# Optimization experiments

Hardware: AMD Instinct MI355X
Metric: run time of the kernel (lower is better)

## Reference

```python
import jax, jax.numpy as jnp
import numpy as np

H = 224; W = 224; ZNEAR = 0.01; ZFAR = 100.0; EPS2D = 0.3
N_GAUSS = 1024; N_CAM = 2
ALPHA_MIN = 1.0 / 255.0; ALPHA_MAX = 0.999


def quat_to_rotmat(q):
    # gsplat convention: wxyz, normalized internally. q: [N,4] -> [N,3,3]
    q = q / jnp.linalg.norm(q, axis=-1, keepdims=True)
    w, x, y, z = q[:, 0], q[:, 1], q[:, 2], q[:, 3]
    R = jnp.stack([
        jnp.stack([1.0 - 2.0 * (y * y + z * z), 2.0 * (x * y - w * z), 2.0 * (x * z + w * y)], -1),
        jnp.stack([2.0 * (x * y + w * z), 1.0 - 2.0 * (x * x + z * z), 2.0 * (y * z - w * x)], -1),
        jnp.stack([2.0 * (x * z - w * y), 2.0 * (y * z + w * x), 1.0 - 2.0 * (x * x + y * y)], -1),
    ], -2)
    return R


def setup_inputs() -> dict:
    key = jax.random.key(0)
    ks = jax.random.split(key, 5)
    xyz = jax.random.normal(ks[0], (N_GAUSS, 3), dtype=jnp.float32) * 0.5
    rgb = jax.random.uniform(ks[1], (N_GAUSS, 3), dtype=jnp.float32)
    opacity = jax.random.uniform(ks[2], (N_GAUSS,), dtype=jnp.float32)
    scale = jax.random.uniform(ks[3], (N_GAUSS, 3), dtype=jnp.float32) * 0.04 + 0.005
    rotation = jax.random.normal(ks[4], (N_GAUSS, 4), dtype=jnp.float32)
    w2c_list = []
    for a in (0.0, 0.3):  # two views, small yaw apart, camera 3 units back
        c, s = np.cos(a), np.sin(a)
        w2c_list.append(np.array([[c, 0, -s, 0], [0, 1, 0, 0], [s, 0, c, 3.0], [0, 0, 0, 1]], dtype=np.float32))
    w2cs = jnp.asarray(np.stack(w2c_list))
    K = np.array([[300.0, 0.0, 112.0], [0.0, 300.0, 112.0], [0.0, 0.0, 1.0]], dtype=np.float32)
    Ks = jnp.asarray(np.stack([K] * N_CAM))
    return {"w2cs": w2cs, "Ks": Ks, "xyz": xyz, "rgb": rgb, "opacity": opacity, "scale": scale, "rotation": rotation}


def _render_one(viewmat, K, means, cov3d, colors, opac, bg):
    R = viewmat[:3, :3]; t = viewmat[:3, 3]
    p_cam = means @ R.T + t                       # [N,3]
    z = p_cam[:, 2]; rz = 1.0 / z
    fx, fy, cx, cy = K[0, 0], K[1, 1], K[0, 2], K[1, 2]
    lim_x = 1.3 * (0.5 * W / fx); lim_y = 1.3 * (0.5 * H / fy)
    tx = z * jnp.clip(p_cam[:, 0] * rz, -lim_x, lim_x)
    ty = z * jnp.clip(p_cam[:, 1] * rz, -lim_y, lim_y)
    # camera-frame 3D covariance, then perspective Jacobian projection to 2D
    cov_cam = jnp.einsum('ij,njk,lk->nil', R, cov3d, R)   # [N,3,3]
    zero = jnp.zeros_like(rz)
    J = jnp.stack([
        jnp.stack([fx * rz, zero, -fx * tx * rz * rz], -1),
        jnp.stack([zero, fy * rz, -fy * ty * rz * rz], -1),
    ], -2)                                                # [N,2,3]
    cov2d = jnp.einsum('nij,njk,nlk->nil', J, cov_cam, J) # [N,2,2]
    a = cov2d[:, 0, 0] + EPS2D; d = cov2d[:, 1, 1] + EPS2D; b = cov2d[:, 0, 1]
    det = a * d - b * b
    ia = d / det; id_ = a / det; ib = -b / det            # inverse of blurred 2D cov
    u = fx * p_cam[:, 0] * rz + cx
    v = fy * p_cam[:, 1] * rz + cy
    valid = (z > ZNEAR) & (z < ZFAR) & (det > 0)
    o = jnp.where(valid, opac, 0.0)
    # front-to-back depth sort (gradients flow through gathered values)
    order = jnp.argsort(z)
    u, v, ia, ib, id_, o = (arr[order] for arr in (u, v, ia, ib, id_, o))
    colors_s = colors[order]
    # pixel centers, row-major flattened grid [P]
    xs = jnp.arange(W, dtype=jnp.float32) + 0.5
    ys = jnp.arange(H, dtype=jnp.float32) + 0.5
    pix_x = jnp.tile(xs, H); pix_y = jnp.repeat(ys, W)
    dx = u[None, :] - pix_x[:, None]                      # [P,N]
    dy = v[None, :] - pix_y[:, None]
    sigma = 0.5 * (ia * dx * dx + id_ * dy * dy) + ib * dx * dy
    alpha = jnp.minimum(o[None, :] * jnp.exp(-sigma), ALPHA_MAX)
    alpha = jnp.where((sigma >= 0.0) & (alpha > ALPHA_MIN), alpha, 0.0)
    log1m = jnp.log1p(-alpha)
    logT = jnp.cumsum(log1m, axis=1)
    T = jnp.exp(logT - log1m)                             # exclusive transmittance
    wgt = alpha * T                                       # [P,N]
    img = wgt @ colors_s                                  # [P,3]
    Tf = jnp.exp(logT[:, -1])
    img = img + Tf[:, None] * bg
    return img.reshape(H, W, 3), (1.0 - Tf).reshape(H, W, 1)


def reference(w2cs, Ks, xyz, rgb, opacity, scale, rotation):
    Rq = quat_to_rotmat(rotation)                         # [N,3,3]
    M = Rq * scale[:, None, :]                            # R @ diag(s)
    cov3d = jnp.einsum('nij,nkj->nik', M, M)              # R S S^T R^T
    bg = jnp.ones((3,), dtype=xyz.dtype)                  # bg_color buffer of ones
    imgs, alphas = jax.vmap(lambda vm, K: _render_one(vm, K, xyz, cov3d, rgb, opacity, bg))(w2cs, Ks)
    return imgs, alphas                                   # rgb [C,H,W,3], mask [C,H,W,1]
```

## Files before the change

kernel.cpp:

```cpp
#include <hip/hip_runtime.h>
#include <math.h>

#define NG 1024
#define NC 2
#define HH 224
#define WW 224
#define TILES_X 28
#define TILES_Y 28
#define EPS2D 0.3f
#define ALPHA_MIN (1.0f/255.0f)
#define ALPHA_MAX 0.999f
#define MAXL 512

__global__ __launch_bounds__(256) void fused_kernel(
        const float* __restrict__ w2cs, const float* __restrict__ Ks,
        const float* __restrict__ xyz, const float* __restrict__ rgb,
        const float* __restrict__ opac, const float* __restrict__ scale,
        const float* __restrict__ rot, float* __restrict__ out) {
    const int cam = blockIdx.z;
    const int TX = blockIdx.x, TY = blockIdx.y;
    const int tid = threadIdx.x;
    const int lane = tid & 63;
    const int wv   = tid >> 6;

    __shared__ unsigned long long keys[MAXL];
    __shared__ float4 sA[MAXL];
    __shared__ float4 sB[MAXL];
    __shared__ float  sC[MAXL];
    __shared__ float4 part[4][64];
    __shared__ int scnt;

    if (tid == 0) scnt = 0;
    __syncthreads();

    const float* vm = w2cs + cam*16;
    const float R00 = vm[0],  R01 = vm[1],  R02 = vm[2],  t0 = vm[3];
    const float R10 = vm[4],  R11 = vm[5],  R12 = vm[6],  t1 = vm[7];
    const float R20 = vm[8],  R21 = vm[9],  R22 = vm[10], t2 = vm[11];
    const float* Kc = Ks + cam*9;
    const float fx = Kc[0], cx = Kc[2], fy = Kc[4], cy = Kc[5];
    const float limx = 1.3f * (0.5f * (float)WW / fx);
    const float limy = 1.3f * (0.5f * (float)HH / fy);

    #pragma unroll
    for (int k = 0; k < 4; k++) {
        int g = k*256 + tid;
        float X = xyz[g*3], Y = xyz[g*3+1], Z = xyz[g*3+2];
        float pz = R20*X + R21*Y + R22*Z + t2;
        float o  = opac[g];
        float tau = __logf(255.f * o);
        bool cand = (pz > 0.01f) && (pz < 100.f) && (tau > 0.f);
        if (cand) {
            float rz = 1.f / pz;
            float px = R00*X + R01*Y + R02*Z + t0;
            float py = R10*X + R11*Y + R12*Z + t1;
            float u = fx*px*rz + cx;
            float v = fy*py*rz + cy;
            float sx = scale[g*3+0], sy = scale[g*3+1], sz = scale[g*3+2];
            float smax = fmaxf(sx, fmaxf(sy, sz));
            float j00 = fx*rz, j11 = fy*rz;
            float j02m = fx*limx*rz, j12m = fy*limy*rz;
            float abnd = smax*smax*(j00*j00 + j02m*j02m) + EPS2D;
            float dbnd = smax*smax*(j11*j11 + j12m*j12m) + EPS2D;
            float rx = sqrtf(2.f*tau*abnd) + 0.01f;
            float ry = sqrtf(2.f*tau*dbnd) + 0.01f;
            int xmin = max((int)ceilf (u - rx - 0.5f), 0);
            int xmax = min((int)floorf(u + rx - 0.5f), WW-1);
            int ymin = max((int)ceilf (v - ry - 0.5f), 0);
            int ymax = min((int)floorf(v + ry - 0.5f), HH-1);
            cand = (xmin <= xmax) && (ymin <= ymax) &&
                   (TX >= (xmin>>3)) && (TX <= (xmax>>3)) &&
                   (TY >= (ymin>>3)) && (TY <= (ymax>>3));
            if (cand) {
                unsigned long long m = __ballot(true);
                (void)m;
            }
        }
        unsigned long long m = __ballot(cand);
        int cw = __popcll(m);
        if (cw) {
            int basepos = 0;
            if (lane == 0) basepos = atomicAdd(&scnt, cw);
            basepos = __shfl(basepos, 0);
            if (cand) {
                float zz = R20*X + R21*Y + R22*Z + t2;
                int pos = basepos + __popcll(m & ((1ull << lane) - 1ull));
                if (pos < MAXL)
                    keys[pos] = ((unsigned long long)__float_as_uint(zz) << 10)
                              | (unsigned long long)g;
            }
        }
    }
    __syncthreads();
    int n = min(scnt, MAXL);

    int P = 2; while (P < n) P <<= 1;
    for (int i = tid; i < P; i += 256) if (i >= n) keys[i] = ~0ull;
    __syncthreads();
    for (int kk = 2; kk <= P; kk <<= 1) {
        for (int j = kk >> 1; j > 0; j >>= 1) {
            for (int i0 = tid; i0 < P; i0 += 256) {
                int ixj = i0 ^ j;
                if (ixj > i0) {
                    unsigned long long a = keys[i0], b = keys[ixj];
                    bool up = ((i0 & kk) == 0);
                    if ((a > b) == up) { keys[i0] = b; keys[ixj] = a; }
                }
            }
            __syncthreads();
        }
    }

    for (int i = tid; i < n; i += 256) {
        int g = (int)(keys[i] & 1023ull);

        float qw = rot[g*4+0], qx = rot[g*4+1], qy = rot[g*4+2], qz = rot[g*4+3];
        float qn = rsqrtf(qw*qw + qx*qx + qy*qy + qz*qz);
        qw *= qn; qx *= qn; qy *= qn; qz *= qn;
        float r00 = 1.f - 2.f*(qy*qy + qz*qz), r01 = 2.f*(qx*qy - qw*qz), r02 = 2.f*(qx*qz + qw*qy);
        float r10 = 2.f*(qx*qy + qw*qz), r11 = 1.f - 2.f*(qx*qx + qz*qz), r12 = 2.f*(qy*qz - qw*qx);
        float r20 = 2.f*(qx*qz - qw*qy), r21 = 2.f*(qy*qz + qw*qx), r22 = 1.f - 2.f*(qx*qx + qy*qy);

        float sx = scale[g*3+0], sy = scale[g*3+1], sz = scale[g*3+2];
        float m00 = r00*sx, m01 = r01*sy, m02 = r02*sz;
        float m10 = r10*sx, m11 = r11*sy, m12 = r12*sz;
        float m20 = r20*sx, m21 = r21*sy, m22 = r22*sz;
        float c00 = m00*m00 + m01*m01 + m02*m02;
        float c01 = m00*m10 + m01*m11 + m02*m12;
        float c02 = m00*m20 + m01*m21 + m02*m22;
        float c11 = m10*m10 + m11*m11 + m12*m12;
        float c12 = m10*m20 + m11*m21 + m12*m22;
        float c22 = m20*m20 + m21*m21 + m22*m22;

        float X = xyz[g*3], Y = xyz[g*3+1], Z = xyz[g*3+2];
        float px = R00*X + R01*Y + R02*Z + t0;
        float py = R10*X + R11*Y + R12*Z + t1;
        float pz = R20*X + R21*Y + R22*Z + t2;
        float rz = 1.f / pz;

        float txc = pz * fminf(fmaxf(px*rz, -limx), limx);
        float tyc = pz * fminf(fmaxf(py*rz, -limy), limy);

        float v00 = R00*c00 + R01*c01 + R02*c02;
        float v01 = R00*c01 + R01*c11 + R02*c12;
        float v02 = R00*c02 + R01*c12 + R02*c22;
        float v10 = R10*c00 + R11*c01 + R12*c02;
        float v11 = R10*c01 + R11*c11 + R12*c12;
        float v12 = R10*c02 + R11*c12 + R12*c22;
        float v20 = R20*c00 + R21*c01 + R22*c02;
        float v21 = R20*c01 + R21*c11 + R22*c12;
        float v22 = R20*c02 + R21*c12 + R22*c22;
        float cc00 = v00*R00 + v01*R01 + v02*R02;
        float cc01 = v00*R10 + v01*R11 + v02*R12;
        float cc02 = v00*R20 + v01*R21 + v02*R22;
        float cc11 = v10*R10 + v11*R11 + v12*R12;
        float cc12 = v10*R20 + v11*R21 + v12*R22;
        float cc22 = v20*R20 + v21*R21 + v22*R22;

        float j00 = fx*rz, j02 = -fx*txc*rz*rz;
        float j11 = fy*rz, j12 = -fy*tyc*rz*rz;
        float a = j00*j00*cc00 + 2.f*j00*j02*cc02 + j02*j02*cc22 + EPS2D;
        float bq = j00*j11*cc01 + j00*j12*cc02 + j02*j11*cc12 + j02*j12*cc22;
        float d = j11*j11*cc11 + 2.f*j11*j12*cc12 + j12*j12*cc22 + EPS2D;
        float det = a*d - bq*bq;

        bool valid = (pz > 0.01f) && (pz < 100.f) && (det > 0.f);
        float idet = valid ? (1.f / det) : 0.f;
        float ia  = d * idet;
        float ib  = -bq * idet;
        float id_ = a * idet;
        float u = valid ? (fx*px*rz + cx) : 0.f;
        float v = valid ? (fy*py*rz + cy) : 0.f;
        float o = valid ? opac[g] : 0.f;

        sA[i] = make_float4(u, v, ia, ib);
        sB[i] = make_float4(id_, o, rgb[g*3+0], rgb[g*3+1]);
        sC[i] = rgb[g*3+2];
    }
    __syncthreads();

    const float pxl = (float)(TX*8 + (lane & 7)) + 0.5f;
    const float pyl = (float)(TY*8 + (lane >> 3)) + 0.5f;
    int seglen = (n + 3) >> 2;
    int js = wv * seglen;
    int je = min(n, js + seglen);

    float T = 1.f, cr = 0.f, cg = 0.f, cb = 0.f;
    for (int j = js; j < je; j++) {
        float4 ga = sA[j];
        float4 gb = sB[j];
        float  bv = sC[j];
        float dx = ga.x - pxl;
        float dy = ga.y - pyl;
        float sigma = 0.5f*(ga.z*dx*dx + gb.x*dy*dy) + ga.w*dx*dy;
        float alpha = fminf(gb.y * __expf(-sigma), ALPHA_MAX);
        alpha = (sigma >= 0.f && alpha > ALPHA_MIN) ? alpha : 0.f;
        float w = alpha * T;
        cr += w * gb.z;
        cg += w * gb.w;
        cb += w * bv;
        T  -= alpha * T;
        if (((j - js) & 15) == 15 && __all(T < 1e-4f)) break;
    }

    part[wv][lane] = make_float4(cr, cg, cb, T);
    __syncthreads();

    if (tid < 64) {
        float4 c0 = part[0][lane];
        float Cr = c0.x, Cg = c0.y, Cb = c0.z, Tp = c0.w;
        #pragma unroll
        for (int s = 1; s < 4; s++) {
            float4 cs = part[s][lane];
            Cr += Tp * cs.x;
            Cg += Tp * cs.y;
            Cb += Tp * cs.z;
            Tp *= cs.w;
        }
        int p = (TY*8 + (lane >> 3)) * WW + TX*8 + (lane & 7);
        float* img = out + (size_t)cam * (HH*WW*3) + (size_t)p * 3;
        img[0] = Cr + Tp;
        img[1] = Cg + Tp;
        img[2] = Cb + Tp;
        out[(size_t)NC*HH*WW*3 + (size_t)cam*(HH*WW) + p] = 1.f - Tp;
    }
}

extern "C" void kernel_launch(void* const* d_in, const int* in_sizes, int n_in,
                              void* d_out, int out_size, void* d_ws, size_t ws_size,
                              hipStream_t stream) {
    const float* w2cs  = (const float*)d_in[0];
    const float* Ks    = (const float*)d_in[1];
    const float* xyz   = (const float*)d_in[2];
    const float* rgb   = (const float*)d_in[3];
    const float* opac  = (const float*)d_in[4];
    const float* scale = (const float*)d_in[5];
    const float* rot   = (const float*)d_in[6];
    float* out = (float*)d_out;

    fused_kernel<<<dim3(TILES_X, TILES_Y, NC), 256, 0, stream>>>(
        w2cs, Ks, xyz, rgb, opac, scale, rot, out);
}
```

Before: 81.00 us.

## Compute full 2D conic per Gaussian before culling and sort slot indices

Each block now computes the full 2D covariance for all 1024 Gaussians up front and uses the exact a/d diagonal for a tighter tile bounding box, instead of a conservative scale-based bound followed by a second pass over the survivors. Preprocessed data is written directly into shared-memory slots, and the sort carries slot indices so the blend loop reads through one indirection. This removes the separate per-survivor preprocessing pass and its sync and culls more Gaussians. In exchange every block does the expensive covariance math for every Gaussian, and the blend loop pays an extra indexed shared-memory load.

```diff
diff --git a/kernel.cpp b/kernel.cpp
--- a/kernel.cpp
+++ b/kernel.cpp
@@ -45,74 +45,6 @@
     #pragma unroll
     for (int k = 0; k < 4; k++) {
         int g = k*256 + tid;
-        float X = xyz[g*3], Y = xyz[g*3+1], Z = xyz[g*3+2];
-        float pz = R20*X + R21*Y + R22*Z + t2;
-        float o  = opac[g];
-        float tau = __logf(255.f * o);
-        bool cand = (pz > 0.01f) && (pz < 100.f) && (tau > 0.f);
-        if (cand) {
-            float rz = 1.f / pz;
-            float px = R00*X + R01*Y + R02*Z + t0;
-            float py = R10*X + R11*Y + R12*Z + t1;
-            float u = fx*px*rz + cx;
-            float v = fy*py*rz + cy;
-            float sx = scale[g*3+0], sy = scale[g*3+1], sz = scale[g*3+2];
-            float smax = fmaxf(sx, fmaxf(sy, sz));
-            float j00 = fx*rz, j11 = fy*rz;
-            float j02m = fx*limx*rz, j12m = fy*limy*rz;
-            float abnd = smax*smax*(j00*j00 + j02m*j02m) + EPS2D;
-            float dbnd = smax*smax*(j11*j11 + j12m*j12m) + EPS2D;
-            float rx = sqrtf(2.f*tau*abnd) + 0.01f;
-            float ry = sqrtf(2.f*tau*dbnd) + 0.01f;
-            int xmin = max((int)ceilf (u - rx - 0.5f), 0);
-            int xmax = min((int)floorf(u + rx - 0.5f), WW-1);
-            int ymin = max((int)ceilf (v - ry - 0.5f), 0);
-            int ymax = min((int)floorf(v + ry - 0.5f), HH-1);
-            cand = (xmin <= xmax) && (ymin <= ymax) &&
-                   (TX >= (xmin>>3)) && (TX <= (xmax>>3)) &&
-                   (TY >= (ymin>>3)) && (TY <= (ymax>>3));
-            if (cand) {
-                unsigned long long m = __ballot(true);
-                (void)m;
-            }
-        }
-        unsigned long long m = __ballot(cand);
-        int cw = __popcll(m);
-        if (cw) {
-            int basepos = 0;
-            if (lane == 0) basepos = atomicAdd(&scnt, cw);
-            basepos = __shfl(basepos, 0);
-            if (cand) {
-                float zz = R20*X + R21*Y + R22*Z + t2;
-                int pos = basepos + __popcll(m & ((1ull << lane) - 1ull));
-                if (pos < MAXL)
-                    keys[pos] = ((unsigned long long)__float_as_uint(zz) << 10)
-                              | (unsigned long long)g;
-            }
-        }
-    }
-    __syncthreads();
-    int n = min(scnt, MAXL);
-
-    int P = 2; while (P < n) P <<= 1;
-    for (int i = tid; i < P; i += 256) if (i >= n) keys[i] = ~0ull;
-    __syncthreads();
-    for (int kk = 2; kk <= P; kk <<= 1) {
-        for (int j = kk >> 1; j > 0; j >>= 1) {
-            for (int i0 = tid; i0 < P; i0 += 256) {
-                int ixj = i0 ^ j;
-                if (ixj > i0) {
-                    unsigned long long a = keys[i0], b = keys[ixj];
-                    bool up = ((i0 & kk) == 0);
-                    if ((a > b) == up) { keys[i0] = b; keys[ixj] = a; }
-                }
-            }
-            __syncthreads();
-        }
-    }
-
-    for (int i = tid; i < n; i += 256) {
-        int g = (int)(keys[i] & 1023ull);
 
         float qw = rot[g*4+0], qx = rot[g*4+1], qy = rot[g*4+2], qz = rot[g*4+3];
         float qn = rsqrtf(qw*qw + qx*qx + qy*qy + qz*qz);
@@ -164,20 +96,63 @@
         float d = j11*j11*cc11 + 2.f*j11*j12*cc12 + j12*j12*cc22 + EPS2D;
         float det = a*d - bq*bq;
 
-        bool valid = (pz > 0.01f) && (pz < 100.f) && (det > 0.f);
-        float idet = valid ? (1.f / det) : 0.f;
-        float ia  = d * idet;
-        float ib  = -bq * idet;
-        float id_ = a * idet;
-        float u = valid ? (fx*px*rz + cx) : 0.f;
-        float v = valid ? (fy*py*rz + cy) : 0.f;
-        float o = valid ? opac[g] : 0.f;
-
-        sA[i] = make_float4(u, v, ia, ib);
-        sB[i] = make_float4(id_, o, rgb[g*3+0], rgb[g*3+1]);
-        sC[i] = rgb[g*3+2];
-    }
-    __syncthreads();
+        float o = opac[g];
+        float tau = __logf(255.f * o);
+        bool cand = (pz > 0.01f) && (pz < 100.f) && (det > 0.f) && (tau > 0.f);
+
+        float u = fx*px*rz + cx;
+        float v = fy*py*rz + cy;
+
+        if (cand) {
+            float rx = sqrtf(2.f * tau * a) + 0.01f;
+            float ry = sqrtf(2.f * tau * d) + 0.01f;
+            int xmin = max((int)ceilf (u - rx - 0.5f), 0);
+            int xmax = min((int)floorf(u + rx - 0.5f), WW-1);
+            int ymin = max((int)ceilf (v - ry - 0.5f), 0);
+            int ymax = min((int)floorf(v + ry - 0.5f), HH-1);
+            cand = (xmin <= xmax) && (ymin <= ymax) &&
+                   (TX >= (xmin>>3)) && (TX <= (xmax>>3)) &&
+                   (TY >= (ymin>>3)) && (TY <= (ymax>>3));
+        }
+
+        unsigned long long m = __ballot(cand);
+        int cw = __popcll(m);
+        if (cw) {
+            int basepos = 0;
+            if (lane == 0) basepos = atomicAdd(&scnt, cw);
+            basepos = __shfl(basepos, 0);
+            if (cand) {
+                int pos = basepos + __popcll(m & ((1ull << lane) - 1ull));
+                if (pos < MAXL) {
+                    float idet = 1.f / det;
+                    keys[pos] = ((unsigned long long)__float_as_uint(pz) << 10)
+                              | (unsigned long long)pos;
+                    sA[pos] = make_float4(u, v, d*idet, -bq*idet);
+                    sB[pos] = make_float4(a*idet, o, rgb[g*3+0], rgb[g*3+1]);
+                    sC[pos] = rgb[g*3+2];
+                }
+            }
+        }
+    }
+    __syncthreads();
+    int n = min(scnt, MAXL);
+
+    int P = 2; while (P < n) P <<= 1;
+    for (int i = tid; i < P; i += 256) if (i >= n) keys[i] = ~0ull;
+    __syncthreads();
+    for (int kk = 2; kk <= P; kk <<= 1) {
+        for (int j = kk >> 1; j > 0; j >>= 1) {
+            for (int i0 = tid; i0 < P; i0 += 256) {
+                int ixj = i0 ^ j;
+                if (ixj > i0) {
+                    unsigned long long a = keys[i0], b = keys[ixj];
+                    bool up = ((i0 & kk) == 0);
+                    if ((a > b) == up) { keys[i0] = b; keys[ixj] = a; }
+                }
+            }
+            __syncthreads();
+        }
+    }
 
     const float pxl = (float)(TX*8 + (lane & 7)) + 0.5f;
     const float pyl = (float)(TY*8 + (lane >> 3)) + 0.5f;
@@ -187,9 +162,10 @@
 
     float T = 1.f, cr = 0.f, cg = 0.f, cb = 0.f;
     for (int j = js; j < je; j++) {
-        float4 ga = sA[j];
-        float4 gb = sB[j];
-        float  bv = sC[j];
+        int slot = (int)(keys[j] & 1023ull);
+        float4 ga = sA[slot];
+        float4 gb = sB[slot];
+        float  bv = sC[slot];
         float dx = ga.x - pxl;
         float dy = ga.y - pyl;
         float sigma = 0.5f*(ga.z*dx*dx + gb.x*dy*dy) + ga.w*dx*dy;
```

Result: slower. 84.44 us (+4.2%).
